# Kernel tuning notes

Measured on AMD Instinct MI355X. Metric: run time of the kernel, lower is better.

The kernel has to match this reference:

```python
import jax, jax.numpy as jnp
import numpy as np

B, N, D = 4, 2048, 1024
WIN, K, ALPHA = 4, 8, 0.3


def setup_inputs() -> dict:
    key = jax.random.key(0)
    ks = jax.random.split(key, 16)
    s_d = 1.0 / np.sqrt(D)
    s_2d = 1.0 / np.sqrt(2 * D)
    inp = {
        'mu': jax.random.normal(ks[0], (B, N, D), jnp.float32),
        'pheromone': jax.random.uniform(ks[1], (B, N), jnp.float32),
        'Wq': jax.random.normal(ks[2], (D, D), jnp.float32) * s_d,
        'bq': jnp.zeros((D,), jnp.float32),
        'Wk': jax.random.normal(ks[3], (D, D), jnp.float32) * s_d,
        'bk': jnp.zeros((D,), jnp.float32),
        'Wv': jax.random.normal(ks[4], (D, D), jnp.float32) * s_d,
        'bv': jnp.zeros((D,), jnp.float32),
        'Wm1': jax.random.normal(ks[5], (2 * D, D), jnp.float32) * s_2d,
        'bm1': jnp.zeros((D,), jnp.float32),
        'Wm2': jax.random.normal(ks[6], (D, D), jnp.float32) * s_d,
        'bm2': jnp.zeros((D,), jnp.float32),
        'Wo': jax.random.normal(ks[7], (2 * D, D), jnp.float32) * s_2d,
        'bo': jnp.zeros((D,), jnp.float32),
    }
    return inp


def reference(mu, pheromone, Wq, bq, Wk, bk, Wv, bv, Wm1, bm1, Wm2, bm2, Wo, bo):
    # ---- local windowed gather-MLP ----
    padded = jnp.pad(mu, ((0, 0), (WIN, 0), (0, 0)))  # causal left-pad
    neighbors = jnp.stack([padded[:, WIN - w:WIN - w + N, :] for w in range(1, WIN + 1)], axis=2)
    self_exp = jnp.broadcast_to(mu[:, :, None, :], neighbors.shape)
    cat = jnp.concatenate([self_exp, neighbors], axis=-1)
    h = jax.nn.silu(cat @ Wm1 + bm1) @ Wm2 + bm2
    local_msgs = h.mean(axis=2)  # (B,N,D)

    # ---- causal top-k attention with pheromone bias ----
    q = mu @ Wq + bq
    k = mu @ Wk + bk
    v = mu @ Wv + bv
    scale = 1.0 / jnp.sqrt(jnp.asarray(D, mu.dtype))
    scores = jnp.einsum('bnd,bmd->bnm', q, k) * scale  # (B,N,N)
    scores = scores + ALPHA * pheromone[:, None, :]
    row = jnp.arange(N)
    causal = jnp.where(row[None, :] > row[:, None], -jnp.inf, 0.0).astype(mu.dtype)
    scores = scores + causal[None]
    # top-k sparsification (N > K): softmax over the k kept scores, zeros elsewhere
    vals, idx = jax.lax.top_k(scores, K)  # (B,N,K)
    probs = jax.nn.softmax(vals, axis=-1)
    bi = jnp.arange(B)[:, None, None]
    ni = jnp.arange(N)[None, :, None]
    attn = jnp.zeros_like(scores).at[bi, ni, idx].set(probs)
    global_msgs = jnp.einsum('bnm,bmd->bnd', attn, v)

    return jnp.concatenate([local_msgs, global_msgs], axis=-1) @ Wo + bo
```

## Files before the change

### kernel.cpp

```cpp
#include <hip/hip_runtime.h>
#include <hip/hip_bf16.h>
#include <math.h>

#define B_ 4
#define N_ 2048
#define D_ 1024
#define WIN_ 4
#define KTOP 8
#define ALPHA_ 0.3f
#define SCALE_ (1.0f/32.0f)
#define NCH 16
#define TROW 36
#define TPLANE (128 * TROW)
#define INV2048 0.00048828125f

typedef unsigned short ushortT;
typedef _Float16 halfT;
typedef __attribute__((ext_vector_type(8))) _Float16 half8v;
typedef __attribute__((ext_vector_type(4))) float f32x4;

__device__ inline ushortT h2u(halfT h){ union{halfT h; ushortT u;} x; x.h=h; return x.u; }
__device__ inline halfT  u2h(ushortT u){ union{halfT h; ushortT u;} x; x.u=u; return x.h; }
__device__ inline float  uh2f(ushortT u){ return (float)u2h(u); }

__global__ __launch_bounds__(256)
void split2_mu(const float* __restrict__ src, ushortT* __restrict__ Pa,
               ushortT* __restrict__ Pb)
{
    size_t base = ((size_t)blockIdx.x * 256 + threadIdx.x) * 4;
    float4 v = *reinterpret_cast<const float4*>(&src[base]);
    float vv[4] = {v.x, v.y, v.z, v.w};
    ushort4 pa, pb;
#pragma unroll
    for (int j = 0; j < 4; ++j) {
        float f = vv[j];
        halfT a = (halfT)f;  float r = f - (float)a;
        halfT b = (halfT)(r * 2048.0f);
        ((ushortT*)&pa)[j] = h2u(a); ((ushortT*)&pb)[j] = h2u(b);
    }
    *reinterpret_cast<ushort4*>(&Pa[base]) = pa;
    *reinterpret_cast<ushort4*>(&Pb[base]) = pb;
}

__global__ __launch_bounds__(256)
void transpose_f2h(const float* __restrict__ W, ushortT* __restrict__ Wt,
                   int K, int Nn)
{
    __shared__ float t[32][33];
    const int k0 = blockIdx.x * 32, n0 = blockIdx.y * 32;
    const int tx = threadIdx.x & 31, ty8 = threadIdx.x >> 5;
#pragma unroll
    for (int p = 0; p < 4; ++p) {
        int kk = p * 8 + ty8;
        t[kk][tx] = W[(size_t)(k0 + kk) * Nn + n0 + tx];
    }
    __syncthreads();
#pragma unroll
    for (int p = 0; p < 4; ++p) {
        int nn = p * 8 + ty8;
        Wt[(size_t)(n0 + nn) * K + k0 + tx] = h2u((halfT)t[tx][nn]);
    }
}

__global__ __launch_bounds__(256)
void transpose_split2(const float* __restrict__ W, ushortT* __restrict__ Pa,
                      ushortT* __restrict__ Pb, int K, int Nn)
{
    __shared__ float t[32][33];
    const int k0 = blockIdx.x * 32, n0 = blockIdx.y * 32;
    const int tx = threadIdx.x & 31, ty8 = threadIdx.x >> 5;
#pragma unroll
    for (int p = 0; p < 4; ++p) {
        int kk = p * 8 + ty8;
        t[kk][tx] = W[(size_t)(k0 + kk) * Nn + n0 + tx];
    }
    __syncthreads();
#pragma unroll
    for (int p = 0; p < 4; ++p) {
        int nn = p * 8 + ty8;
        float f = t[tx][nn];
        halfT a = (halfT)f;  float r = f - (float)a;
        halfT b = (halfT)(r * 2048.0f);
        size_t o = (size_t)(n0 + nn) * K + k0 + tx;
        Pa[o] = h2u(a); Pb[o] = h2u(b);
    }
}

template<int OUT_HALF>
__global__ __launch_bounds__(256)
void mfma_gemm_h(const ushortT* __restrict__ A, int lda,
                 const ushortT* __restrict__ Bt, int ldb,
                 const float* __restrict__ bias,
                 void* __restrict__ Cout, int ldc, int K)
{
    __shared__ ushortT AsL[128 * 72];
    __shared__ ushortT BsL[128 * 72];
    const int tid = threadIdx.x;
    const int m0 = blockIdx.y * 128;
    const int n0 = blockIdx.x * 128;
    const int w = tid >> 6, lane = tid & 63;
    const int wr = w >> 1, wc = w & 1;

    f32x4 acc[4][4];
#pragma unroll
    for (int mi = 0; mi < 4; ++mi)
#pragma unroll
        for (int ni = 0; ni < 4; ++ni) acc[mi][ni] = (f32x4){0.f, 0.f, 0.f, 0.f};

    for (int k0 = 0; k0 < K; k0 += 64) {
#pragma unroll
        for (int it = 0; it < 4; ++it) {
            int idx = tid + it * 256;
            int row = idx >> 3, c = idx & 7;
            int4 va = *reinterpret_cast<const int4*>(&A[(size_t)(m0 + row) * lda + k0 + c * 8]);
            *reinterpret_cast<int4*>(&AsL[row * 72 + c * 8]) = va;
            int4 vb = *reinterpret_cast<const int4*>(&Bt[(size_t)(n0 + row) * ldb + k0 + c * 8]);
            *reinterpret_cast<int4*>(&BsL[row * 72 + c * 8]) = vb;
        }
        __syncthreads();
#pragma unroll
        for (int kh = 0; kh < 2; ++kh) {
            const int ko = kh * 32 + (lane >> 4) * 8;
            const int rr = lane & 15;
            half8v af[4], bf[4];
#pragma unroll
            for (int mi = 0; mi < 4; ++mi)
                af[mi] = *reinterpret_cast<const half8v*>(&AsL[(wr * 64 + mi * 16 + rr) * 72 + ko]);
#pragma unroll
            for (int ni = 0; ni < 4; ++ni)
                bf[ni] = *reinterpret_cast<const half8v*>(&BsL[(wc * 64 + ni * 16 + rr) * 72 + ko]);
#pragma unroll
            for (int mi = 0; mi < 4; ++mi)
#pragma unroll
                for (int ni = 0; ni < 4; ++ni)
                    acc[mi][ni] = __builtin_amdgcn_mfma_f32_16x16x32_f16(
                        af[mi], bf[ni], acc[mi][ni], 0, 0, 0);
        }
        __syncthreads();
    }

    const int r4 = (lane >> 4) * 4, cl = lane & 15;
#pragma unroll
    for (int mi = 0; mi < 4; ++mi)
#pragma unroll
        for (int ni = 0; ni < 4; ++ni) {
            int row = m0 + wr * 64 + mi * 16 + r4;
            int col = n0 + wc * 64 + ni * 16 + cl;
            float bb = bias ? bias[col] : 0.f;
#pragma unroll
            for (int r = 0; r < 4; ++r) {
                float v = acc[mi][ni][r] + bb;
                if (OUT_HALF)
                    ((ushortT*)Cout)[(size_t)(row + r) * ldc + col] = h2u((halfT)v);
                else
                    ((float*)Cout)[(size_t)(row + r) * ldc + col] = v;
            }
        }
}

__global__ __launch_bounds__(256)
void silu_mean(const float* __restrict__ P, const float* __restrict__ bm1,
               ushortT* __restrict__ Sb)
{
    size_t idx4 = (size_t)blockIdx.x * blockDim.x + threadIdx.x;
    size_t base = idx4 << 2;
    int row = (int)(base >> 10);
    int col = (int)(base & 1023);
    int n = row & (N_ - 1);
    float4 a = *reinterpret_cast<const float4*>(&P[(size_t)row * 2048 + col]);
    float4 bb = *reinterpret_cast<const float4*>(&bm1[col]);
    a.x += bb.x; a.y += bb.y; a.z += bb.z; a.w += bb.w;
    float sx = 0.f, sy = 0.f, sz = 0.f, sw = 0.f;
#pragma unroll
    for (int w = 1; w <= WIN_; ++w) {
        float xx = a.x, xy = a.y, xz = a.z, xw = a.w;
        if (n >= w) {
            const float4 nb = *reinterpret_cast<const float4*>(
                &P[(size_t)(row - w) * 2048 + 1024 + col]);
            xx += nb.x; xy += nb.y; xz += nb.z; xw += nb.w;
        }
        sx += xx / (1.f + __expf(-xx));
        sy += xy / (1.f + __expf(-xy));
        sz += xz / (1.f + __expf(-xz));
        sw += xw / (1.f + __expf(-xw));
    }
    ushort4 o = {h2u((halfT)(sx * 0.25f)), h2u((halfT)(sy * 0.25f)),
                 h2u((halfT)(sz * 0.25f)), h2u((halfT)(sw * 0.25f))};
    *reinterpret_cast<ushort4*>(&Sb[base]) = o;
}

__device__ inline void topk_insert(float (&tv)[KTOP], int (&ti)[KTOP], float s, int m)
{
    if ((s > tv[KTOP-1]) || (s == tv[KTOP-1] && m < ti[KTOP-1])) {
        float cs = s; int ci = m;
#pragma unroll
        for (int q = 0; q < KTOP; ++q) {
            bool beats = (cs > tv[q]) || (cs == tv[q] && ci < ti[q]);
            if (beats) { float t0 = tv[q]; int t1 = ti[q];
                         tv[q] = cs; ti[q] = ci; cs = t0; ci = t1; }
        }
    }
}

#define SPLIT3H_COMPUTE(T4, wr, wc, lane, acc0, acc1)                           \
    {                                                                           \
        const int rr_ = (lane) & 15, ko_ = ((lane) >> 4) * 8;                   \
        half8v ba0_ = *reinterpret_cast<const half8v*>(                         \
            &T4[2 * TPLANE + ((wc) * 32 + rr_) * TROW + ko_]);                  \
        half8v ba1_ = *reinterpret_cast<const half8v*>(                         \
            &T4[2 * TPLANE + ((wc) * 32 + 16 + rr_) * TROW + ko_]);             \
        half8v bB0_ = *reinterpret_cast<const half8v*>(                         \
            &T4[3 * TPLANE + ((wc) * 32 + rr_) * TROW + ko_]);                  \
        half8v bB1_ = *reinterpret_cast<const half8v*>(                         \
            &T4[3 * TPLANE + ((wc) * 32 + 16 + rr_) * TROW + ko_]);             \
        _Pragma("unroll")                                                       \
        for (int mi_ = 0; mi_ < 4; ++mi_) {                                     \
            half8v aA_ = *reinterpret_cast<const half8v*>(                      \
                &T4[0 * TPLANE + ((wr) * 64 + mi_ * 16 + rr_) * TROW + ko_]);   \
            acc0[mi_][0] = __builtin_amdgcn_mfma_f32_16x16x32_f16(              \
                aA_, ba0_, acc0[mi_][0], 0, 0, 0);                              \
            acc0[mi_][1] = __builtin_amdgcn_mfma_f32_16x16x32_f16(              \
                aA_, ba1_, acc0[mi_][1], 0, 0, 0);                              \
            acc1[mi_][0] = __builtin_amdgcn_mfma_f32_16x16x32_f16(              \
                aA_, bB0_, acc1[mi_][0], 0, 0, 0);                              \
            acc1[mi_][1] = __builtin_amdgcn_mfma_f32_16x16x32_f16(              \
                aA_, bB1_, acc1[mi_][1], 0, 0, 0);                              \
        }                                                                       \
        _Pragma("unroll")                                                       \
        for (int mi_ = 0; mi_ < 4; ++mi_) {                                     \
            half8v aB_ = *reinterpret_cast<const half8v*>(                      \
                &T4[1 * TPLANE + ((wr) * 64 + mi_ * 16 + rr_) * TROW + ko_]);   \
            acc1[mi_][0] = __builtin_amdgcn_mfma_f32_16x16x32_f16(              \
                aB_, ba0_, acc1[mi_][0], 0, 0, 0);                              \
            acc1[mi_][1] = __builtin_amdgcn_mfma_f32_16x16x32_f16(              \
                aB_, ba1_, acc1[mi_][1], 0, 0, 0);                              \
        }                                                                       \
    }

__global__ __launch_bounds__(512, 4)
void gemm_split3h(const ushortT* __restrict__ A0, const ushortT* __restrict__ A1,
                  const ushortT* __restrict__ B0, const ushortT* __restrict__ B1,
                  const float* __restrict__ bias,
                  ushortT* __restrict__ Pa, ushortT* __restrict__ Pb)
{
    __shared__ ushortT T4[4 * TPLANE];

    int lin = blockIdx.y * 8 + blockIdx.x;
    lin = (lin & 7) * 64 + (lin >> 3);
    const int m0 = (lin >> 3) * 128;
    const int n0 = (lin & 7) * 128;

    const int tid = threadIdx.x;
    const int wid = tid >> 6, lane = tid & 63;
    const int wr = wid >> 2, wc = wid & 3;
    const int rowL = tid >> 2, cL = tid & 3;

    const size_t offA = (size_t)(m0 + rowL) * D_ + cL * 8;
    const size_t offB = (size_t)(n0 + rowL) * D_ + cL * 8;
    const int ldst = rowL * TROW + cL * 8;

    f32x4 acc0[4][2], acc1[4][2];
#pragma unroll
    for (int mi = 0; mi < 4; ++mi) {
        acc0[mi][0] = (f32x4){0,0,0,0}; acc0[mi][1] = (f32x4){0,0,0,0};
        acc1[mi][0] = (f32x4){0,0,0,0}; acc1[mi][1] = (f32x4){0,0,0,0};
    }

    int4 s0, s1, s2, s3;
    s0 = *reinterpret_cast<const int4*>(&A0[offA]);
    s1 = *reinterpret_cast<const int4*>(&A1[offA]);
    s2 = *reinterpret_cast<const int4*>(&B0[offB]);
    s3 = *reinterpret_cast<const int4*>(&B1[offB]);

    for (int ks = 0; ks < 32; ++ks) {
        __syncthreads();
        *reinterpret_cast<int4*>(&T4[0 * TPLANE + ldst]) = s0;
        *reinterpret_cast<int4*>(&T4[1 * TPLANE + ldst]) = s1;
        *reinterpret_cast<int4*>(&T4[2 * TPLANE + ldst]) = s2;
        *reinterpret_cast<int4*>(&T4[3 * TPLANE + ldst]) = s3;
        __syncthreads();
        if (ks < 31) {
            const int kk = (ks + 1) * 32;
            s0 = *reinterpret_cast<const int4*>(&A0[offA + kk]);
            s1 = *reinterpret_cast<const int4*>(&A1[offA + kk]);
            s2 = *reinterpret_cast<const int4*>(&B0[offB + kk]);
            s3 = *reinterpret_cast<const int4*>(&B1[offB + kk]);
        }
        __builtin_amdgcn_s_setprio(1);
        SPLIT3H_COMPUTE(T4, wr, wc, lane, acc0, acc1)
        __builtin_amdgcn_s_setprio(0);
    }

    const int r4 = (lane >> 4) * 4, cl = lane & 15;
#pragma unroll
    for (int mi = 0; mi < 4; ++mi)
#pragma unroll
        for (int ni = 0; ni < 2; ++ni) {
            int col = n0 + wc * 32 + ni * 16 + cl;
            float bb = bias[col];
#pragma unroll
            for (int r = 0; r < 4; ++r) {
                int row = m0 + wr * 64 + mi * 16 + r4 + r;
                float v = acc0[mi][ni][r] + INV2048 * acc1[mi][ni][r] + bb;
                halfT a = (halfT)v;  float r1 = v - (float)a;
                halfT b = (halfT)(r1 * 2048.0f);
                size_t o = (size_t)row * D_ + col;
                Pa[o] = h2u(a); Pb[o] = h2u(b);
            }
        }
}

__global__ __launch_bounds__(512, 4)
void attn_scores_h(const ushortT* __restrict__ Qa, const ushortT* __restrict__ QB,
                   const ushortT* __restrict__ Ka, const ushortT* __restrict__ KB,
                   const float* __restrict__ pher,
                   float* __restrict__ WV, int* __restrict__ WI)
{
    __shared__ ushortT T4[4 * TPLANE];
    __shared__ float Ps[128];
    __shared__ float PV[32 * 4 * 8];
    __shared__ int   PI[32 * 4 * 8];
    float* MV = reinterpret_cast<float*>(&T4[0]);
    int*   MI = reinterpret_cast<int*>((char*)&T4[0] + 16384);

    int lin = blockIdx.y * 136 + blockIdx.x;
    lin = (lin & 7) * 68 + (lin >> 3);
    const int b = lin / 136;
    const int xy = lin - b * 136;
    int g = 0;
    while ((g + 1) * (g + 2) / 2 <= xy) ++g;
    const int ch = xy - g * (g + 1) / 2;
    const int n0 = g * 128;
    const int m0 = ch * 128;
    const size_t bN = (size_t)b * N_;

    const int tid = threadIdx.x;
    const int wid = tid >> 6, lane = tid & 63;
    const int wr = wid >> 2, wc = wid & 3;
    const int rowL = tid >> 2, cL = tid & 3;

    if (tid < 128) Ps[tid] = pher[bN + m0 + tid];

    const size_t offQ = (bN + n0 + rowL) * (size_t)D_ + cL * 8;
    const size_t offK = (bN + m0 + rowL) * (size_t)D_ + cL * 8;
    const int ldst = rowL * TROW + cL * 8;

    f32x4 acc0[4][2], acc1[4][2];
#pragma unroll
    for (int mi = 0; mi < 4; ++mi) {
        acc0[mi][0] = (f32x4){0,0,0,0}; acc0[mi][1] = (f32x4){0,0,0,0};
        acc1[mi][0] = (f32x4){0,0,0,0}; acc1[mi][1] = (f32x4){0,0,0,0};
    }

    int4 s0, s1, s2, s3;
    s0 = *reinterpret_cast<const int4*>(&Qa[offQ]);
    s1 = *reinterpret_cast<const int4*>(&QB[offQ]);
    s2 = *reinterpret_cast<const int4*>(&Ka[offK]);
    s3 = *reinterpret_cast<const int4*>(&KB[offK]);

    for (int ks = 0; ks < 32; ++ks) {
        __syncthreads();
        *reinterpret_cast<int4*>(&T4[0 * TPLANE + ldst]) = s0;
        *reinterpret_cast<int4*>(&T4[1 * TPLANE + ldst]) = s1;
        *reinterpret_cast<int4*>(&T4[2 * TPLANE + ldst]) = s2;
        *reinterpret_cast<int4*>(&T4[3 * TPLANE + ldst]) = s3;
        __syncthreads();
        if (ks < 31) {
            const int kk = (ks + 1) * 32;
            s0 = *reinterpret_cast<const int4*>(&Qa[offQ + kk]);
            s1 = *reinterpret_cast<const int4*>(&QB[offQ + kk]);
            s2 = *reinterpret_cast<const int4*>(&Ka[offK + kk]);
            s3 = *reinterpret_cast<const int4*>(&KB[offK + kk]);
        }
        __builtin_amdgcn_s_setprio(1);
        SPLIT3H_COMPUTE(T4, wr, wc, lane, acc0, acc1)
        __builtin_amdgcn_s_setprio(0);
    }

    const int r4 = (lane >> 4) * 4, cl = lane & 15;
    for (int p = 0; p < 4; ++p) {
        __syncthreads();
        if (wr == (p >> 1)) {
#pragma unroll
            for (int mi2 = 0; mi2 < 2; ++mi2) {
                const int mi = (p & 1) * 2 + mi2;
#pragma unroll
                for (int ni = 0; ni < 2; ++ni) {
                    int col = wc * 32 + ni * 16 + cl;
                    int m = m0 + col;
#pragma unroll
                    for (int r = 0; r < 4; ++r) {
                        int rloc = mi2 * 16 + r4 + r;
                        int n = n0 + p * 32 + rloc;
                        bool ok = (m <= n);
                        float sc = acc0[mi][ni][r] + INV2048 * acc1[mi][ni][r];
                        MV[rloc * 128 + col] = ok ? (sc * SCALE_ + ALPHA_ * Ps[col])
                                                  : -INFINITY;
                        MI[rloc * 128 + col] = ok ? m : 0x7fffffff;
                    }
                }
            }
        }
        __syncthreads();
        if (tid < 128) {
            const int row = tid >> 2, q4 = tid & 3;
            float tv[KTOP]; int ti[KTOP];
#pragma unroll
            for (int j = 0; j < KTOP; ++j) { tv[j] = -INFINITY; ti[j] = 0x7fffffff; }
            for (int j = 0; j < 32; ++j) {
                float s2 = MV[row * 128 + q4 * 32 + j];
                if (s2 == -INFINITY) continue;
                topk_insert(tv, ti, s2, MI[row * 128 + q4 * 32 + j]);
            }
#pragma unroll
            for (int j = 0; j < KTOP; ++j) {
                PV[(row * 4 + q4) * 8 + j] = tv[j];
                PI[(row * 4 + q4) * 8 + j] = ti[j];
            }
        }
        __syncthreads();
        if (tid < 32) {
            float tv[KTOP]; int ti[KTOP];
#pragma unroll
            for (int j = 0; j < KTOP; ++j) { tv[j] = -INFINITY; ti[j] = 0x7fffffff; }
            for (int i = 0; i < 32; ++i) {
                float s2 = PV[tid * 32 + i];
                if (s2 == -INFINITY) continue;
                topk_insert(tv, ti, s2, PI[tid * 32 + i]);
            }
            int n = n0 + p * 32 + tid;
            size_t base = ((bN + n) * NCH + ch) * 8;
#pragma unroll
            for (int j = 0; j < KTOP; ++j) { WV[base + j] = tv[j]; WI[base + j] = ti[j]; }
        }
    }
}

__global__ __launch_bounds__(256)
void attn_merge(const float* __restrict__ WV, const int* __restrict__ WI,
                const ushortT* __restrict__ V, ushortT* __restrict__ CCb)
{
    __shared__ float CV[4][128];
    __shared__ int   CI[4][128];
    __shared__ float Pp[4][KTOP];
    __shared__ int   Pi[4][KTOP];

    const int tid  = threadIdx.x;
    const int wv   = tid >> 6;
    const int lane = tid & 63;
    const int rid  = blockIdx.x * 4 + wv;
    const int b    = rid >> 11;
    const int n    = rid & (N_ - 1);
    const int ncand = ((n >> 7) + 1) * 8;
    const size_t cbase = (size_t)rid * (NCH * 8);

#pragma unroll
    for (int t = 0; t < 2; ++t) {
        int i = lane + t * 64;
        if (i < ncand) { CV[wv][i] = WV[cbase + i]; CI[wv][i] = WI[cbase + i]; }
        else           { CV[wv][i] = -INFINITY;     CI[wv][i] = 0x7fffffff;   }
    }
    __syncthreads();

    if (lane == 0) {
        float tv[KTOP]; int ti[KTOP];
#pragma unroll
        for (int j = 0; j < KTOP; ++j) { tv[j] = -INFINITY; ti[j] = 0x7fffffff; }
        for (int i = 0; i < 128; ++i) {
            float s = CV[wv][i];
            if (s == -INFINITY) continue;
            topk_insert(tv, ti, s, CI[wv][i]);
        }
        float mx = tv[0];
        float e[KTOP]; float sum = 0.f;
#pragma unroll
        for (int j = 0; j < KTOP; ++j) {
            e[j] = (tv[j] == -INFINITY) ? 0.f : __expf(tv[j] - mx);
            sum += e[j];
        }
        float inv = 1.f / sum;
#pragma unroll
        for (int j = 0; j < KTOP; ++j) {
            Pp[wv][j] = e[j] * inv;
            Pi[wv][j] = (tv[j] == -INFINITY) ? 0 : ti[j];
        }
    }
    __syncthreads();

    const size_t vbase = (size_t)b * N_ * D_;
#pragma unroll
    for (int it = 0; it < 2; ++it) {
        int c8 = (it * 64 + lane) * 8;
        float o[8];
#pragma unroll
        for (int u = 0; u < 8; ++u) o[u] = 0.f;
#pragma unroll
        for (int j = 0; j < KTOP; ++j) {
            float p = Pp[wv][j];
            ushort4 v0 = *reinterpret_cast<const ushort4*>(
                &V[vbase + (size_t)Pi[wv][j] * D_ + c8]);
            ushort4 v1 = *reinterpret_cast<const ushort4*>(
                &V[vbase + (size_t)Pi[wv][j] * D_ + c8 + 4]);
            o[0] = fmaf(p, uh2f(v0.x), o[0]); o[1] = fmaf(p, uh2f(v0.y), o[1]);
            o[2] = fmaf(p, uh2f(v0.z), o[2]); o[3] = fmaf(p, uh2f(v0.w), o[3]);
            o[4] = fmaf(p, uh2f(v1.x), o[4]); o[5] = fmaf(p, uh2f(v1.y), o[5]);
            o[6] = fmaf(p, uh2f(v1.z), o[6]); o[7] = fmaf(p, uh2f(v1.w), o[7]);
        }
        ushort4 ob0 = {h2u((halfT)o[0]), h2u((halfT)o[1]), h2u((halfT)o[2]), h2u((halfT)o[3])};
        ushort4 ob1 = {h2u((halfT)o[4]), h2u((halfT)o[5]), h2u((halfT)o[6]), h2u((halfT)o[7])};
        *reinterpret_cast<ushort4*>(&CCb[(size_t)rid * 2048 + 1024 + c8]) = ob0;
        *reinterpret_cast<ushort4*>(&CCb[(size_t)rid * 2048 + 1024 + c8 + 4]) = ob1;
    }
}

extern "C" void kernel_launch(void* const* d_in, const int* in_sizes, int n_in,
                              void* d_out, int out_size, void* d_ws, size_t ws_size,
                              hipStream_t stream)
{
    const float* mu   = (const float*)d_in[0];
    const float* pher = (const float*)d_in[1];
    const float* Wq   = (const float*)d_in[2];
    const float* bq   = (const float*)d_in[3];
    const float* Wk   = (const float*)d_in[4];
    const float* bk   = (const float*)d_in[5];
    const float* Wv   = (const float*)d_in[6];
    const float* bv   = (const float*)d_in[7];
    const float* Wm1  = (const float*)d_in[8];
    const float* bm1  = (const float*)d_in[9];
    const float* Wm2  = (const float*)d_in[10];
    const float* bm2  = (const float*)d_in[11];
    const float* Wo   = (const float*)d_in[12];
    const float* bo   = (const float*)d_in[13];
    float* out = (float*)d_out;
    float* ws  = (float*)d_ws;

    const size_t SZ  = (size_t)B_ * N_ * D_;
    const size_t MEG = 1024 * 1024;
    const int M = B_ * N_;

    ushortT* CCb  = (ushortT*)ws;
    float*   PF   = ws + SZ;
    ushortT* Qa   = (ushortT*)(ws + SZ);
    ushortT* QB   = Qa + SZ;
    ushortT* Ka   = (ushortT*)(ws + 2 * SZ);
    ushortT* KB   = Ka + SZ;
    ushortT* mu_a = (ushortT*)(ws + 3 * SZ);
    ushortT* mu_B = mu_a + SZ;
    ushortT* Sb   = (ushortT*)(ws + 4 * SZ);
    float*   WVb  = (float*)(ws + 4 * SZ);
    int*     WIb  = (int*)(WVb + MEG);
    ushortT* Vb16 = (ushortT*)(ws + 4 * SZ + 2 * MEG);
    ushortT* U    = (ushortT*)(ws + 4 * SZ + 2 * MEG + SZ / 2);
    ushortT* WtF  = U;
    ushortT* Wt_m2 = U + 2 * MEG;
    ushortT* Wt_v  = U + 3 * MEG;
    ushortT* WqT_a = U + 4 * MEG;        ushortT* WqT_B = U + 5 * MEG;
    ushortT* WkT_a = U + 6 * MEG;        ushortT* WkT_B = U + 7 * MEG;
    ushortT* Wt_o  = U + 8 * MEG;

    dim3 blk256(256), blk512(512);
    dim3 gD(8, 64);

    hipLaunchKernelGGL(split2_mu, dim3(SZ / 8 / 128), blk256, 0, stream, mu, mu_a, mu_B);
    hipLaunchKernelGGL(transpose_f2h, dim3(32, 32), blk256, 0, stream, Wm1, WtF, 1024, 1024);
    hipLaunchKernelGGL(transpose_f2h, dim3(32, 32), blk256, 0, stream,
                       Wm1 + (size_t)1024 * 1024, WtF + (size_t)1024 * 1024, 1024, 1024);
    hipLaunchKernelGGL(transpose_f2h, dim3(32, 32), blk256, 0, stream, Wm2, Wt_m2, 1024, 1024);
    hipLaunchKernelGGL(transpose_f2h, dim3(32, 32), blk256, 0, stream, Wv, Wt_v, 1024, 1024);
    hipLaunchKernelGGL(transpose_f2h, dim3(64, 32), blk256, 0, stream, Wo, Wt_o, 2048, 1024);
    hipLaunchKernelGGL(transpose_split2, dim3(32, 32), blk256, 0, stream,
                       Wq, WqT_a, WqT_B, 1024, 1024);
    hipLaunchKernelGGL(transpose_split2, dim3(32, 32), blk256, 0, stream,
                       Wk, WkT_a, WkT_B, 1024, 1024);
    hipLaunchKernelGGL((mfma_gemm_h<0>), dim3(16, 64), blk256, 0, stream,
                       mu_a, D_, WtF, D_, (const float*)nullptr, (void*)PF, 2 * D_, D_);
    hipLaunchKernelGGL(silu_mean, dim3(SZ / 4 / 256), blk256, 0, stream, PF, bm1, Sb);
    hipLaunchKernelGGL((mfma_gemm_h<1>), gD, blk256, 0, stream,
                       Sb, D_, Wt_m2, D_, bm2, (void*)CCb, 2 * D_, D_);
    hipLaunchKernelGGL((mfma_gemm_h<1>), gD, blk256, 0, stream,
                       mu_a, D_, Wt_v, D_, bv, (void*)Vb16, D_, D_);
    hipLaunchKernelGGL(gemm_split3h, gD, blk512, 0, stream,
                       mu_a, mu_B, WqT_a, WqT_B, bq, Qa, QB);
    hipLaunchKernelGGL(gemm_split3h, gD, blk512, 0, stream,
                       mu_a, mu_B, WkT_a, WkT_B, bk, Ka, KB);
    hipLaunchKernelGGL(attn_scores_h, dim3(136, B_), blk512, 0, stream,
                       Qa, QB, Ka, KB, pher, WVb, WIb);
    hipLaunchKernelGGL(attn_merge, dim3(M / 4), blk256, 0, stream, WVb, WIb, Vb16, CCb);
    hipLaunchKernelGGL((mfma_gemm_h<0>), gD, blk256, 0, stream,
                       CCb, 2 * D_, Wt_o, 2048, bo, (void*)out, D_, 2 * D_);

    (void)in_sizes; (void)n_in; (void)out_size; (void)ws_size;
}
```

Before: 775.5 us.

## Use direct global-to-LDS loads with double buffering and XOR swizzle in split GEMMs

The projection GEMM and attention-score kernels now stage tiles with global_load_lds (16-byte direct global-to-LDS copies) into two LDS buffers instead of a register round-trip. This allows one barrier per k-step, with the next tile loading while MFMAs run on the current one. Padded rows are replaced by an XOR-swizzled layout to avoid bank conflicts. Doubling LDS use lowers the occupancy hint from 4 to 2 blocks per CU, which could reduce latency hiding.

```diff
diff --git a/kernel.cpp b/kernel.cpp
--- a/kernel.cpp
+++ b/kernel.cpp
@@ -10,8 +10,6 @@
 #define ALPHA_ 0.3f
 #define SCALE_ (1.0f/32.0f)
 #define NCH 16
-#define TROW 36
-#define TPLANE (128 * TROW)
 #define INV2048 0.00048828125f
 
 typedef unsigned short ushortT;
@@ -22,6 +20,12 @@
 __device__ inline ushortT h2u(halfT h){ union{halfT h; ushortT u;} x; x.h=h; return x.u; }
 __device__ inline halfT  u2h(ushortT u){ union{halfT h; ushortT u;} x; x.u=u; return x.h; }
 __device__ inline float  uh2f(ushortT u){ return (float)u2h(u); }
+
+__device__ __forceinline__ void gll16(const ushortT* g, ushortT* l) {
+    __builtin_amdgcn_global_load_lds(
+        (const __attribute__((address_space(1))) void*)g,
+        (__attribute__((address_space(3))) void*)l, 16, 0, 0);
+}
 
 __global__ __launch_bounds__(256)
 void split2_mu(const float* __restrict__ src, ushortT* __restrict__ Pa,
@@ -202,21 +206,24 @@
     }
 }
 
-#define SPLIT3H_COMPUTE(T4, wr, wc, lane, acc0, acc1)                           \
+#define SPLIT3H_COMPUTE(Tb, wr, wc, lane, acc0, acc1)                           \
     {                                                                           \
-        const int rr_ = (lane) & 15, ko_ = ((lane) >> 4) * 8;                   \
+        const int rr_ = (lane) & 15, q_ = (lane) >> 4;                          \
+        const int Rb0_ = (wc) * 32 + rr_;                                       \
+        const int Rb1_ = Rb0_ + 16;                                             \
         half8v ba0_ = *reinterpret_cast<const half8v*>(                         \
-            &T4[2 * TPLANE + ((wc) * 32 + rr_) * TROW + ko_]);                  \
+            &Tb[2 * 4096 + Rb0_ * 32 + ((q_ ^ ((Rb0_ >> 1) & 3)) << 3)]);       \
         half8v ba1_ = *reinterpret_cast<const half8v*>(                         \
-            &T4[2 * TPLANE + ((wc) * 32 + 16 + rr_) * TROW + ko_]);             \
+            &Tb[2 * 4096 + Rb1_ * 32 + ((q_ ^ ((Rb1_ >> 1) & 3)) << 3)]);       \
         half8v bB0_ = *reinterpret_cast<const half8v*>(                         \
-            &T4[3 * TPLANE + ((wc) * 32 + rr_) * TROW + ko_]);                  \
+            &Tb[3 * 4096 + Rb0_ * 32 + ((q_ ^ ((Rb0_ >> 1) & 3)) << 3)]);       \
         half8v bB1_ = *reinterpret_cast<const half8v*>(                         \
-            &T4[3 * TPLANE + ((wc) * 32 + 16 + rr_) * TROW + ko_]);             \
+            &Tb[3 * 4096 + Rb1_ * 32 + ((q_ ^ ((Rb1_ >> 1) & 3)) << 3)]);       \
         _Pragma("unroll")                                                       \
         for (int mi_ = 0; mi_ < 4; ++mi_) {                                     \
-            half8v aA_ = *reinterpret_cast<const half8v*>(                      \
-                &T4[0 * TPLANE + ((wr) * 64 + mi_ * 16 + rr_) * TROW + ko_]);   \
+            const int Ra_ = (wr) * 64 + mi_ * 16 + rr_;                         \
+            const int sw_ = (q_ ^ ((Ra_ >> 1) & 3)) << 3;                       \
+            half8v aA_ = *reinterpret_cast<const half8v*>(&Tb[Ra_ * 32 + sw_]); \
             acc0[mi_][0] = __builtin_amdgcn_mfma_f32_16x16x32_f16(              \
                 aA_, ba0_, acc0[mi_][0], 0, 0, 0);                              \
             acc0[mi_][1] = __builtin_amdgcn_mfma_f32_16x16x32_f16(              \
@@ -228,8 +235,10 @@
         }                                                                       \
         _Pragma("unroll")                                                       \
         for (int mi_ = 0; mi_ < 4; ++mi_) {                                     \
+            const int Ra_ = (wr) * 64 + mi_ * 16 + rr_;                         \
+            const int sw_ = (q_ ^ ((Ra_ >> 1) & 3)) << 3;                       \
             half8v aB_ = *reinterpret_cast<const half8v*>(                      \
-                &T4[1 * TPLANE + ((wr) * 64 + mi_ * 16 + rr_) * TROW + ko_]);   \
+                &Tb[4096 + Ra_ * 32 + sw_]);                                    \
             acc1[mi_][0] = __builtin_amdgcn_mfma_f32_16x16x32_f16(              \
                 aB_, ba0_, acc1[mi_][0], 0, 0, 0);                              \
             acc1[mi_][1] = __builtin_amdgcn_mfma_f32_16x16x32_f16(              \
@@ -237,13 +246,21 @@
         }                                                                       \
     }
 
-__global__ __launch_bounds__(512, 4)
+#define STAGE4(lb, koff)                                                        \
+    {                                                                           \
+        gll16(gp + goff + (koff), lb);                                          \
+        gll16(gp + goff + (koff) + 16 * D_, (lb) + 512);                        \
+        gll16(gp + goff + (koff) + 32 * D_, (lb) + 1024);                       \
+        gll16(gp + goff + (koff) + 48 * D_, (lb) + 1536);                       \
+    }
+
+__global__ __launch_bounds__(512, 2)
 void gemm_split3h(const ushortT* __restrict__ A0, const ushortT* __restrict__ A1,
                   const ushortT* __restrict__ B0, const ushortT* __restrict__ B1,
                   const float* __restrict__ bias,
                   ushortT* __restrict__ Pa, ushortT* __restrict__ Pb)
 {
-    __shared__ ushortT T4[4 * TPLANE];
+    __shared__ ushortT TT[2][16384];
 
     int lin = blockIdx.y * 8 + blockIdx.x;
     lin = (lin & 7) * 64 + (lin >> 3);
@@ -253,11 +270,15 @@
     const int tid = threadIdx.x;
     const int wid = tid >> 6, lane = tid & 63;
     const int wr = wid >> 2, wc = wid & 3;
-    const int rowL = tid >> 2, cL = tid & 3;
-
-    const size_t offA = (size_t)(m0 + rowL) * D_ + cL * 8;
-    const size_t offB = (size_t)(n0 + rowL) * D_ + cL * 8;
-    const int ldst = rowL * TROW + cL * 8;
+
+    const int pl = wid >> 1;
+    const int hb = (wid & 1) * 64;
+    const ushortT* gp = (pl == 0) ? A0 : (pl == 1) ? A1 : (pl == 2) ? B0 : B1;
+    const int rbase = (pl < 2 ? m0 : n0) + hb + (lane >> 2);
+    const int cg8 = ((lane & 3) ^ ((lane >> 3) & 3)) << 3;
+    const size_t goff = (size_t)rbase * D_ + cg8;
+    ushortT* lb0 = &TT[0][pl * 4096 + hb * 32];
+    ushortT* lb1 = &TT[1][pl * 4096 + hb * 32];
 
     f32x4 acc0[4][2], acc1[4][2];
 #pragma unroll
@@ -266,29 +287,21 @@
         acc1[mi][0] = (f32x4){0,0,0,0}; acc1[mi][1] = (f32x4){0,0,0,0};
     }
 
-    int4 s0, s1, s2, s3;
-    s0 = *reinterpret_cast<const int4*>(&A0[offA]);
-    s1 = *reinterpret_cast<const int4*>(&A1[offA]);
-    s2 = *reinterpret_cast<const int4*>(&B0[offB]);
-    s3 = *reinterpret_cast<const int4*>(&B1[offB]);
-
+    STAGE4(lb0, 0)
+    __syncthreads();
+
+    int cur = 0;
     for (int ks = 0; ks < 32; ++ks) {
+        if (ks < 31) {
+            ushortT* lb = cur ? lb0 : lb1;
+            STAGE4(lb, (size_t)(ks + 1) * 32)
+        }
+        const ushortT* Tb = &TT[cur][0];
+        __builtin_amdgcn_s_setprio(1);
+        SPLIT3H_COMPUTE(Tb, wr, wc, lane, acc0, acc1)
+        __builtin_amdgcn_s_setprio(0);
         __syncthreads();
-        *reinterpret_cast<int4*>(&T4[0 * TPLANE + ldst]) = s0;
-        *reinterpret_cast<int4*>(&T4[1 * TPLANE + ldst]) = s1;
-        *reinterpret_cast<int4*>(&T4[2 * TPLANE + ldst]) = s2;
-        *reinterpret_cast<int4*>(&T4[3 * TPLANE + ldst]) = s3;
-        __syncthreads();
-        if (ks < 31) {
-            const int kk = (ks + 1) * 32;
-            s0 = *reinterpret_cast<const int4*>(&A0[offA + kk]);
-            s1 = *reinterpret_cast<const int4*>(&A1[offA + kk]);
-            s2 = *reinterpret_cast<const int4*>(&B0[offB + kk]);
-            s3 = *reinterpret_cast<const int4*>(&B1[offB + kk]);
-        }
-        __builtin_amdgcn_s_setprio(1);
-        SPLIT3H_COMPUTE(T4, wr, wc, lane, acc0, acc1)
-        __builtin_amdgcn_s_setprio(0);
+        cur ^= 1;
     }
 
     const int r4 = (lane >> 4) * 4, cl = lane & 15;
@@ -310,18 +323,18 @@
         }
 }
 
-__global__ __launch_bounds__(512, 4)
+__global__ __launch_bounds__(512, 2)
 void attn_scores_h(const ushortT* __restrict__ Qa, const ushortT* __restrict__ QB,
                    const ushortT* __restrict__ Ka, const ushortT* __restrict__ KB,
                    const float* __restrict__ pher,
                    float* __restrict__ WV, int* __restrict__ WI)
 {
-    __shared__ ushortT T4[4 * TPLANE];
+    __shared__ ushortT TT[2][16384];
     __shared__ float Ps[128];
     __shared__ float PV[32 * 4 * 8];
     __shared__ int   PI[32 * 4 * 8];
-    float* MV = reinterpret_cast<float*>(&T4[0]);
-    int*   MI = reinterpret_cast<int*>((char*)&T4[0] + 16384);
+    float* MV = reinterpret_cast<float*>(&TT[0][0]);
+    int*   MI = reinterpret_cast<int*>((char*)&TT[0][0] + 16384);
 
     int lin = blockIdx.y * 136 + blockIdx.x;
     lin = (lin & 7) * 68 + (lin >> 3);
@@ -337,13 +350,17 @@
     const int tid = threadIdx.x;
     const int wid = tid >> 6, lane = tid & 63;
     const int wr = wid >> 2, wc = wid & 3;
-    const int rowL = tid >> 2, cL = tid & 3;
 
     if (tid < 128) Ps[tid] = pher[bN + m0 + tid];
 
-    const size_t offQ = (bN + n0 + rowL) * (size_t)D_ + cL * 8;
-    const size_t offK = (bN + m0 + rowL) * (size_t)D_ + cL * 8;
-    const int ldst = rowL * TROW + cL * 8;
+    const int pl = wid >> 1;
+    const int hb = (wid & 1) * 64;
+    const ushortT* gp = (pl == 0) ? Qa : (pl == 1) ? QB : (pl == 2) ? Ka : KB;
+    const size_t rbase = bN + (pl < 2 ? n0 : m0) + hb + (lane >> 2);
+    const int cg8 = ((lane & 3) ^ ((lane >> 3) & 3)) << 3;
+    const size_t goff = rbase * (size_t)D_ + cg8;
+    ushortT* lb0 = &TT[0][pl * 4096 + hb * 32];
+    ushortT* lb1 = &TT[1][pl * 4096 + hb * 32];
 
     f32x4 acc0[4][2], acc1[4][2];
 #pragma unroll
@@ -352,29 +369,21 @@
         acc1[mi][0] = (f32x4){0,0,0,0}; acc1[mi][1] = (f32x4){0,0,0,0};
     }
 
-    int4 s0, s1, s2, s3;
-    s0 = *reinterpret_cast<const int4*>(&Qa[offQ]);
-    s1 = *reinterpret_cast<const int4*>(&QB[offQ]);
-    s2 = *reinterpret_cast<const int4*>(&Ka[offK]);
-    s3 = *reinterpret_cast<const int4*>(&KB[offK]);
-
+    STAGE4(lb0, 0)
+    __syncthreads();
+
+    int cur = 0;
     for (int ks = 0; ks < 32; ++ks) {
+        if (ks < 31) {
+            ushortT* lb = cur ? lb0 : lb1;
+            STAGE4(lb, (size_t)(ks + 1) * 32)
+        }
+        const ushortT* Tb = &TT[cur][0];
+        __builtin_amdgcn_s_setprio(1);
+        SPLIT3H_COMPUTE(Tb, wr, wc, lane, acc0, acc1)
+        __builtin_amdgcn_s_setprio(0);
         __syncthreads();
-        *reinterpret_cast<int4*>(&T4[0 * TPLANE + ldst]) = s0;
-        *reinterpret_cast<int4*>(&T4[1 * TPLANE + ldst]) = s1;
-        *reinterpret_cast<int4*>(&T4[2 * TPLANE + ldst]) = s2;
-        *reinterpret_cast<int4*>(&T4[3 * TPLANE + ldst]) = s3;
-        __syncthreads();
-        if (ks < 31) {
-            const int kk = (ks + 1) * 32;
-            s0 = *reinterpret_cast<const int4*>(&Qa[offQ + kk]);
-            s1 = *reinterpret_cast<const int4*>(&QB[offQ + kk]);
-            s2 = *reinterpret_cast<const int4*>(&Ka[offK + kk]);
-            s3 = *reinterpret_cast<const int4*>(&KB[offK + kk]);
-        }
-        __builtin_amdgcn_s_setprio(1);
-        SPLIT3H_COMPUTE(T4, wr, wc, lane, acc0, acc1)
-        __builtin_amdgcn_s_setprio(0);
+        cur ^= 1;
     }
 
     const int r4 = (lane >> 4) * 4, cl = lane & 15;
```

Result: faster. 757.5 us (-2.3%).
